# Optimization experiments

Measured on AMD Instinct MI355X. Metric: run time of the kernel, lower is better.

The kernel has to match this reference:

```python
import jax, jax.numpy as jnp
import numpy as np

D_MODEL = 1024
N_HEAD = 16
D_K = 64
D_V = 64
D_INNER = 4096
MAX_REL = 16
EPS = 1e-6


def _rel_index(length_q, length_k):
    # Shaw-style clipped relative distance matrix -> indices into embedding table
    dist = jnp.arange(length_k)[None, :] - jnp.arange(length_q)[:, None]
    return jnp.clip(dist, -MAX_REL, MAX_REL) + MAX_REL  # [Lq, Lk] in [0, 2*MAX_REL]


def _layer_norm(x, gamma, beta):
    mu = jnp.mean(x, axis=-1, keepdims=True)
    var = jnp.var(x, axis=-1, keepdims=True)
    return (x - mu) / jnp.sqrt(var + EPS) * gamma + beta


def setup_inputs() -> dict:
    key = jax.random.key(0)
    ks = jax.random.split(key, 16)
    B, L = 8, 1024
    s = 0.02
    inp = {
        "q": jax.random.normal(ks[0], (B, L, D_MODEL), jnp.float32),
        "k": jax.random.normal(ks[1], (B, L, D_MODEL), jnp.float32),
        "v": jax.random.normal(ks[2], (B, L, D_MODEL), jnp.float32),
        "wq": jax.random.normal(ks[3], (D_MODEL, D_MODEL), jnp.float32) * s,
        "bq": jnp.zeros((D_MODEL,), jnp.float32),
        "wk": jax.random.normal(ks[4], (D_MODEL, D_MODEL), jnp.float32) * s,
        "bk": jnp.zeros((D_MODEL,), jnp.float32),
        "wv": jax.random.normal(ks[5], (D_MODEL, D_MODEL), jnp.float32) * s,
        "bv": jnp.zeros((D_MODEL,), jnp.float32),
        "wfc": jax.random.normal(ks[6], (D_MODEL, D_MODEL), jnp.float32) * s,
        "bfc": jnp.zeros((D_MODEL,), jnp.float32),
        "w1": jax.random.normal(ks[7], (D_MODEL, D_INNER), jnp.float32) * s,
        "b1": jnp.zeros((D_INNER,), jnp.float32),
        "w2": jax.random.normal(ks[8], (D_INNER, D_MODEL), jnp.float32) * s,
        "b2": jnp.zeros((D_MODEL,), jnp.float32),
        "ln_g": jnp.ones((D_MODEL,), jnp.float32),
        "ln_b": jnp.zeros((D_MODEL,), jnp.float32),
        "rel_k": jax.random.normal(ks[9], (2 * MAX_REL + 1, D_K), jnp.float32) * s,
        "rel_v": jax.random.normal(ks[10], (2 * MAX_REL + 1, D_V), jnp.float32) * s,
    }
    return inp


def reference(q, k, v, wq, bq, wk, bk, wv, bv, wfc, bfc, w1, b1, w2, b2, ln_g, ln_b, rel_k, rel_v):
    B, Lq, _ = q.shape
    Lk = k.shape[1]
    residual = q

    Q = q @ wq + bq  # [B, Lq, D]
    K = k @ wk + bk
    V = v @ wv + bv

    Qh = Q.reshape(B, Lq, N_HEAD, D_K)  # [B, Lq, H, dk]
    Kh = K.reshape(B, Lk, N_HEAD, D_K)
    Vh = V.reshape(B, Lk, N_HEAD, D_V)

    # content-content scores
    attn1 = jnp.einsum("bqhd,bkhd->bhqk", Qh, Kh)
    # content-position scores (Shaw relative position)
    idx = _rel_index(Lq, Lk)  # [Lq, Lk]
    k2 = rel_k[idx]           # [Lq, Lk, dk]
    attn2 = jnp.einsum("bqhd,qkd->bhqk", Qh, k2)

    attn = (attn1 + attn2) / jnp.sqrt(jnp.float32(D_K))
    attn = jax.nn.softmax(attn, axis=-1)  # dropout = identity (eval)

    weight1 = jnp.einsum("bhqk,bkhd->bhqd", attn, Vh)
    v2 = rel_v[idx]  # [Lq, Lk, dv]
    weight2 = jnp.einsum("bhqk,qkd->bhqd", attn, v2)

    out = (weight1 + weight2).transpose(0, 2, 1, 3).reshape(B, Lq, N_HEAD * D_V)
    out = out @ wfc + bfc
    out = out + residual
    out = _layer_norm(out, ln_g, ln_b)

    residual = out
    out2 = jax.nn.relu(out @ w1 + b1) @ w2 + b2
    out = _layer_norm(out2 + residual, ln_g, ln_b)  # same LN params reused, as in source
    return out
```

## Files before the change

kernel.cpp:

```cpp
#include <hip/hip_runtime.h>
#include <stdint.h>


typedef __bf16 bf16x8 __attribute__((ext_vector_type(8)));
typedef float  f32x4  __attribute__((ext_vector_type(4)));

__device__ __forceinline__ unsigned short f2bf(float f) {
  __bf16 h = (__bf16)f;
  union { __bf16 h; unsigned short u; } x; x.h = h;
  return x.u;
}
__device__ __forceinline__ float bf2f(unsigned short h) {
  union { unsigned u; float f; } x; x.u = ((unsigned)h) << 16; return x.f;
}

__device__ __forceinline__ void gload_lds16(
    const unsigned short* g,
    __attribute__((address_space(3))) unsigned int* l) {
  __builtin_amdgcn_global_load_lds(
      (const __attribute__((address_space(1))) unsigned int*)g, l, 16, 0, 0);
}

template<int EPI>
__global__ __launch_bounds__(512, 2) void gemm_bt(
    const unsigned short* __restrict__ A,
    const unsigned short* __restrict__ Bt,
    const float* __restrict__ bias0,
    const float* __restrict__ bias1,
    const float* __restrict__ bias2,
    void* __restrict__ Cout,
    int M, int N, int K,
    size_t sA, size_t sB, size_t sC)
{
  __shared__ __align__(16) unsigned short S[3 * 24576];
  const int tid = threadIdx.x;
  const int lane = tid & 63, wv = tid >> 6;
  const int lq = lane >> 4, lm = lane & 15;
  const int wr = wv >> 2, wc = wv & 3;

  const int z = blockIdx.z;
  const float* bias = (z == 0) ? bias0 : (z == 1) ? bias1 : bias2;
  A  += (size_t)z * sA;
  Bt += (size_t)z * sB;

  const int nx = gridDim.x;
  const int nwg = nx * gridDim.y;
  int bid = blockIdx.y * nx + blockIdx.x;
  bid = (bid & 7) * (nwg >> 3) + (bid >> 3);
  const int m0 = (bid / nx) * 256, n0 = (bid % nx) * 128;

  const int srow = tid >> 3;
  const int scol = ((tid & 7) ^ (srow & 7)) * 8;
  const unsigned short* ga = A  + (size_t)(m0 + srow) * K + scol;
  const unsigned short* gb = Bt + (size_t)(n0 + srow) * K + scol;

  __attribute__((address_space(3))) unsigned int* lbase =
      (__attribute__((address_space(3))) unsigned int*)S;

  f32x4 acc[8][2] = {};

  auto stage = [&](int buf) {
    __attribute__((address_space(3))) unsigned int* lA = lbase + buf * 12288 + wv * 256;
    __attribute__((address_space(3))) unsigned int* lB = lA + 8192;
    #pragma unroll
    for (int g = 0; g < 4; ++g)
      gload_lds16(ga + (size_t)(g * 64) * K, lA + g * 2048);
    #pragma unroll
    for (int g = 0; g < 2; ++g)
      gload_lds16(gb + (size_t)(g * 64) * K, lB + g * 2048);
    ga += 64; gb += 64;
  };

  const int csw0 = ((lq ^ (lm & 7)) << 4);
  const int csw1 = csw0 ^ 64;
  const char* fa = (const char*)S + (wr * 128 + lm) * 128;
  const char* fb = (const char*)S + 32768 + (wc * 32 + lm) * 128;

  auto compute_tile = [&](int buf) {
    const char* ba = fa + buf * 49152;
    const char* bb = fb + buf * 49152;
    bf16x8 bfr[2][2];
    #pragma unroll
    for (int j = 0; j < 2; ++j) {
      bfr[j][0] = *(const bf16x8*)(bb + j * 2048 + csw0);
      bfr[j][1] = *(const bf16x8*)(bb + j * 2048 + csw1);
    }
    #pragma unroll
    for (int q = 0; q < 4; ++q) {
      bf16x8 af[2][2];
      #pragma unroll
      for (int ii = 0; ii < 2; ++ii) {
        af[ii][0] = *(const bf16x8*)(ba + (q * 2 + ii) * 2048 + csw0);
        af[ii][1] = *(const bf16x8*)(ba + (q * 2 + ii) * 2048 + csw1);
      }
      __builtin_amdgcn_s_barrier();
      __builtin_amdgcn_s_setprio(1);
      #pragma unroll
      for (int ii = 0; ii < 2; ++ii)
        #pragma unroll
        for (int j = 0; j < 2; ++j)
          #pragma unroll
          for (int kk = 0; kk < 2; ++kk)
            acc[q * 2 + ii][j] = __builtin_amdgcn_mfma_f32_16x16x32_bf16(
                af[ii][kk], bfr[j][kk], acc[q * 2 + ii][j], 0, 0, 0);
      __builtin_amdgcn_s_setprio(0);
      __builtin_amdgcn_s_barrier();
    }
  };

  const int nt = K >> 6;
  stage(0);
  stage(1);
  for (int t = 0; t < nt; ++t) {
    if (t + 1 < nt) asm volatile("s_waitcnt vmcnt(6)" ::: "memory");
    else            asm volatile("s_waitcnt vmcnt(0)" ::: "memory");
    __builtin_amdgcn_s_barrier();
    __builtin_amdgcn_sched_barrier(0);
    if (t + 2 < nt) stage((t + 2) % 3);
    compute_tile(t % 3);
  }

  #pragma unroll
  for (int i = 0; i < 8; ++i) {
    #pragma unroll
    for (int j = 0; j < 2; ++j) {
      const int col = n0 + wc * 32 + j * 16 + lm;
      const float bv = bias[col];
      #pragma unroll
      for (int r = 0; r < 4; ++r) {
        const int row = m0 + wr * 128 + i * 16 + lq * 4 + r;
        float v = acc[i][j][r] + bv;
        if (EPI == 2) v = fmaxf(v, 0.0f);
        if (EPI == 1) ((float*)Cout)[(size_t)row * N + col] = v;
        else ((unsigned short*)Cout + (size_t)z * sC)[(size_t)row * N + col] = f2bf(v);
      }
    }
  }
}

__global__ __launch_bounds__(256) void tcast(
    const float* __restrict__ in, unsigned short* __restrict__ out, int R, int C)
{
  __shared__ float tile[32][33];
  const int tx = threadIdx.x & 31, ty = threadIdx.x >> 5;
  const int r0 = blockIdx.y * 32, c0 = blockIdx.x * 32;
  #pragma unroll
  for (int s = 0; s < 4; ++s)
    tile[ty + s * 8][tx] = in[(size_t)(r0 + ty + s * 8) * C + c0 + tx];
  __syncthreads();
  #pragma unroll
  for (int s = 0; s < 4; ++s)
    out[(size_t)(c0 + ty + s * 8) * R + r0 + tx] = f2bf(tile[tx][ty + s * 8]);
}

__global__ __launch_bounds__(256) void cast4(
    const float* __restrict__ in, unsigned short* __restrict__ out, int n)
{
  int i = (blockIdx.x * 256 + threadIdx.x) * 4;
  if (i < n) {
    float4 v = *(const float4*)(in + i);
    ushort4 o;
    o.x = f2bf(v.x); o.y = f2bf(v.y); o.z = f2bf(v.z); o.w = f2bf(v.w);
    *(ushort4*)(out + i) = o;
  }
}

__global__ __launch_bounds__(256) void vtrans(
    const unsigned short* __restrict__ VP, unsigned short* __restrict__ VPT)
{
  __shared__ unsigned short tile[64 * 66];
  const int pt = blockIdx.x, h = blockIdx.y, b = blockIdx.z;
  const int tid = threadIdx.x;
  const int p = tid >> 2, c0 = (tid & 3) * 16;
  const unsigned short* src = VP + (size_t)(b * 1024 + pt * 64 + p) * 1024 + h * 64 + c0;
  union { uint4 q; unsigned int u[4]; } t0, t1;
  t0.q = *(const uint4*)src;
  t1.q = *(const uint4*)(src + 8);
  #pragma unroll
  for (int e = 0; e < 4; ++e) {
    *(unsigned int*)&tile[p * 66 + c0 + e * 2]     = t0.u[e];
    *(unsigned int*)&tile[p * 66 + c0 + 8 + e * 2] = t1.u[e];
  }
  __syncthreads();
  const int d = tid >> 2, p0 = (tid & 3) * 16;
  union { uint4 q[2]; unsigned short s[16]; } ob;
  #pragma unroll
  for (int e = 0; e < 16; ++e) ob.s[e] = tile[(p0 + e) * 66 + d];
  unsigned short* dst = VPT + ((size_t)(h * 64 + d) * 8 + b) * 1024 + pt * 64 + p0;
  *(uint4*)dst       = ob.q[0];
  *(uint4*)(dst + 8) = ob.q[1];
}

__global__ __launch_bounds__(256, 4) void attn_flash(
    const unsigned short* __restrict__ Qp,
    const unsigned short* __restrict__ Kp,
    const unsigned short* __restrict__ VPT,
    const float* __restrict__ relk,
    const float* __restrict__ relv,
    unsigned short* __restrict__ ctx)
{
  int id = (blockIdx.z * gridDim.y + blockIdx.y) * gridDim.x + blockIdx.x;
  id = (id & 7) * 256 + (id >> 3);
  const int qt = id & 15, h = (id >> 4) & 15, b = id >> 8;

  const int tid = threadIdx.x;
  const int lane = tid & 63, wv = tid >> 6;
  const int lq = lane >> 4, lm = lane & 15;

  __shared__ __align__(16) unsigned short SM[18560];
  unsigned short* Kt    = SM;
  unsigned short* Vt    = SM + 4608;
  unsigned short* Pt    = SM + 9216;
  unsigned short* RaccB = SM + 13824;
  unsigned short* qrelB = SM + 16384;
  unsigned short* relvT = SM;

  const float CE = 0.125f * 1.44269504088896340736f;

  const int tok0 = b * 1024 + qt * 64;

  for (int i = tid; i < 64 * 40; i += 256) RaccB[i] = 0;

  bf16x8 qf0, qf1;
  {
    const unsigned short* qg = Qp + (size_t)(tok0 + wv * 16 + lm) * 1024 + h * 64;
    qf0 = *(const bf16x8*)(qg + lq * 8);
    qf1 = *(const bf16x8*)(qg + 32 + lq * 8);
  }

  #pragma unroll
  for (int t = 0; t < 3; ++t) {
    const int bin = t * 16 + lm;
    union { bf16x8 v; unsigned short s[8]; } rk0, rk1;
    #pragma unroll
    for (int e = 0; e < 8; ++e) { rk0.s[e] = 0; rk1.s[e] = 0; }
    if (bin < 33) {
      const float* rp = relk + bin * 64 + lq * 8;
      #pragma unroll
      for (int e = 0; e < 8; ++e) {
        rk0.s[e] = f2bf(rp[e]);
        rk1.s[e] = f2bf(rp[32 + e]);
      }
    }
    f32x4 Sr = {};
    Sr = __builtin_amdgcn_mfma_f32_16x16x32_bf16(qf0, rk0.v, Sr, 0, 0, 0);
    Sr = __builtin_amdgcn_mfma_f32_16x16x32_bf16(qf1, rk1.v, Sr, 0, 0, 0);
    if (bin < 33) {
      #pragma unroll
      for (int r = 0; r < 4; ++r)
        qrelB[(wv * 16 + lq * 4 + r) * 34 + bin] = f2bf(Sr[r] * CE);
    }
  }
  __syncthreads();

  float q0a[4], q32a[4];
  #pragma unroll
  for (int r = 0; r < 4; ++r) {
    const int rowl = wv * 16 + lq * 4 + r;
    q0a[r]  = bf2f(qrelB[rowl * 34 + 0]);
    q32a[r] = bf2f(qrelB[rowl * 34 + 32]);
  }

  union { bf16x8 v; unsigned short s[8]; } one8;
  #pragma unroll
  for (int e = 0; e < 8; ++e) one8.s[e] = 0x3F80;

  f32x4 Oa[4] = {};
  f32x4 Rs = {};
  float r0a[4] = {0, 0, 0, 0}, r32a[4] = {0, 0, 0, 0};

  const int srow = tid >> 2, scol = (tid & 3) * 16;
  const unsigned short* kg = Kp + (size_t)(b * 1024 + srow) * 1024 + h * 64 + scol;
  const unsigned short* vg = VPT + ((size_t)(h * 64 + srow) * 8 + b) * 1024 + scol;
  const int qa0 = qt * 64 + wv * 16;

  uint4 rk0_ = *(const uint4*)(kg);
  uint4 rk1_ = *(const uint4*)(kg + 8);
  uint4 rv0_ = *(const uint4*)(vg);
  uint4 rv1_ = *(const uint4*)(vg + 8);

  for (int kt = 0; kt < 16; ++kt) {
    __syncthreads();
    *(uint4*)(Kt + srow * 72 + scol)     = rk0_;
    *(uint4*)(Kt + srow * 72 + scol + 8) = rk1_;
    *(uint4*)(Vt + srow * 72 + scol)     = rv0_;
    *(uint4*)(Vt + srow * 72 + scol + 8) = rv1_;
    if (kt < 15) {
      kg += 64 * 1024;
      vg += 64;
      rk0_ = *(const uint4*)(kg);
      rk1_ = *(const uint4*)(kg + 8);
      rv0_ = *(const uint4*)(vg);
      rv1_ = *(const uint4*)(vg + 8);
    }
    __syncthreads();

    #pragma unroll
    for (int tj = 0; tj < 4; ++tj) {
      bf16x8 kf0 = *(const bf16x8*)(Kt + (tj * 16 + lm) * 72 + lq * 8);
      bf16x8 kf1 = *(const bf16x8*)(Kt + (tj * 16 + lm) * 72 + 32 + lq * 8);
      f32x4 S = {};
      S = __builtin_amdgcn_mfma_f32_16x16x32_bf16(qf0, kf0, S, 0, 0, 0);
      S = __builtin_amdgcn_mfma_f32_16x16x32_bf16(qf1, kf1, S, 0, 0, 0);
      const int c0 = kt * 64 + tj * 16;
      if (c0 + 31 <= qa0) {
        #pragma unroll
        for (int r = 0; r < 4; ++r) {
          const float p = __builtin_amdgcn_exp2f(fmaf(S[r], CE, q0a[r]));
          r0a[r] += p;
          Pt[(wv * 16 + lq * 4 + r) * 72 + tj * 16 + lm] = f2bf(p);
        }
      } else if (c0 >= qa0 + 31) {
        #pragma unroll
        for (int r = 0; r < 4; ++r) {
          const float p = __builtin_amdgcn_exp2f(fmaf(S[r], CE, q32a[r]));
          r32a[r] += p;
          Pt[(wv * 16 + lq * 4 + r) * 72 + tj * 16 + lm] = f2bf(p);
        }
      } else {
        const int kpos = c0 + lm;
        #pragma unroll
        for (int r = 0; r < 4; ++r) {
          const int rowl = wv * 16 + lq * 4 + r;
          const int dist = kpos - (qt * 64 + rowl);
          const int bin = (dist < -16 ? 0 : (dist > 16 ? 32 : dist + 16));
          const float p =
              __builtin_amdgcn_exp2f(fmaf(S[r], CE, bf2f(qrelB[rowl * 34 + bin])));
          if (bin == 0)       r0a[r]  += p;
          else if (bin == 32) r32a[r] += p;
          else RaccB[rowl * 40 + bin] = f2bf(p);
          Pt[rowl * 72 + tj * 16 + lm] = f2bf(p);
        }
      }
    }
    bf16x8 pf0 = *(const bf16x8*)(Pt + (wv * 16 + lm) * 72 + lq * 8);
    bf16x8 pf1 = *(const bf16x8*)(Pt + (wv * 16 + lm) * 72 + 32 + lq * 8);
    Rs = __builtin_amdgcn_mfma_f32_16x16x32_bf16(pf0, one8.v, Rs, 0, 0, 0);
    Rs = __builtin_amdgcn_mfma_f32_16x16x32_bf16(pf1, one8.v, Rs, 0, 0, 0);
    #pragma unroll
    for (int dt = 0; dt < 4; ++dt) {
      bf16x8 vf0 = *(const bf16x8*)(Vt + (dt * 16 + lm) * 72 + lq * 8);
      bf16x8 vf1 = *(const bf16x8*)(Vt + (dt * 16 + lm) * 72 + 32 + lq * 8);
      Oa[dt] = __builtin_amdgcn_mfma_f32_16x16x32_bf16(pf0, vf0, Oa[dt], 0, 0, 0);
      Oa[dt] = __builtin_amdgcn_mfma_f32_16x16x32_bf16(pf1, vf1, Oa[dt], 0, 0, 0);
    }
  }

  #pragma unroll
  for (int r = 0; r < 4; ++r) {
    #pragma unroll
    for (int off = 1; off < 16; off <<= 1) {
      r0a[r]  += __shfl_xor(r0a[r],  off, 64);
      r32a[r] += __shfl_xor(r32a[r], off, 64);
    }
  }
  if (lm == 0) {
    #pragma unroll
    for (int r = 0; r < 4; ++r)
      RaccB[(wv * 16 + lq * 4 + r) * 40 + 0] = f2bf(r0a[r]);
  }
  __syncthreads();
  for (int i = tid; i < 64 * 32; i += 256) {
    const int dd = i >> 5, ss = i & 31;
    relvT[dd * 32 + ss] = f2bf(relv[ss * 64 + dd]);
  }
  __syncthreads();

  bf16x8 raf = *(const bf16x8*)(RaccB + (wv * 16 + lm) * 40 + lq * 8);
  #pragma unroll
  for (int dt = 0; dt < 4; ++dt) {
    bf16x8 rvb = *(const bf16x8*)(relvT + (dt * 16 + lm) * 32 + lq * 8);
    f32x4 O2 = {};
    O2 = __builtin_amdgcn_mfma_f32_16x16x32_bf16(raf, rvb, O2, 0, 0, 0);
    const float rv32 = relv[32 * 64 + dt * 16 + lm];
    #pragma unroll
    for (int r = 0; r < 4; ++r) {
      const int rowl = wv * 16 + lq * 4 + r;
      const float v = (Oa[dt][r] + O2[r] + r32a[r] * rv32) / Rs[r];
      ctx[(size_t)(tok0 + rowl) * 1024 + h * 64 + dt * 16 + lm] = f2bf(v);
    }
  }
}

template<bool WB>
__global__ __launch_bounds__(256) void ln_res(
    const float* __restrict__ x, const float* __restrict__ res,
    const float* __restrict__ g, const float* __restrict__ bta,
    float* __restrict__ of, unsigned short* __restrict__ ob)
{
  const int row = blockIdx.x;
  const int tid = threadIdx.x;
  __shared__ float red[8];
  const size_t base = (size_t)row * 1024 + tid * 4;
  const float4 xv = *(const float4*)(x + base);
  const float4 rv = *(const float4*)(res + base);
  float v0 = xv.x + rv.x, v1 = xv.y + rv.y, v2 = xv.z + rv.z, v3 = xv.w + rv.w;
  float s1 = v0 + v1 + v2 + v3;
  float s2 = v0 * v0 + v1 * v1 + v2 * v2 + v3 * v3;
  #pragma unroll
  for (int off = 1; off < 64; off <<= 1) {
    s1 += __shfl_xor(s1, off, 64);
    s2 += __shfl_xor(s2, off, 64);
  }
  const int wv = tid >> 6;
  if ((tid & 63) == 0) { red[wv * 2] = s1; red[wv * 2 + 1] = s2; }
  __syncthreads();
  s1 = red[0] + red[2] + red[4] + red[6];
  s2 = red[1] + red[3] + red[5] + red[7];
  const float mean = s1 * (1.f / 1024.f);
  const float var = s2 * (1.f / 1024.f) - mean * mean;
  const float rstd = rsqrtf(var + 1e-6f);
  const float4 gv = *(const float4*)(g + tid * 4);
  const float4 bv = *(const float4*)(bta + tid * 4);
  float y0 = (v0 - mean) * rstd * gv.x + bv.x;
  float y1 = (v1 - mean) * rstd * gv.y + bv.y;
  float y2 = (v2 - mean) * rstd * gv.z + bv.z;
  float y3 = (v3 - mean) * rstd * gv.w + bv.w;
  float4 yo; yo.x = y0; yo.y = y1; yo.z = y2; yo.w = y3;
  *(float4*)(of + base) = yo;
  if (WB) {
    ushort4 o;
    o.x = f2bf(y0); o.y = f2bf(y1); o.z = f2bf(y2); o.w = f2bf(y3);
    *(ushort4*)(ob + base) = o;
  }
}

extern "C" void kernel_launch(void* const* d_in, const int* in_sizes, int n_in,
                              void* d_out, int out_size, void* d_ws, size_t ws_size,
                              hipStream_t stream) {
  (void)in_sizes; (void)n_in; (void)out_size; (void)ws_size;
  const float* q    = (const float*)d_in[0];
  const float* k    = (const float*)d_in[1];
  const float* v    = (const float*)d_in[2];
  const float* wq   = (const float*)d_in[3];
  const float* bq   = (const float*)d_in[4];
  const float* wk   = (const float*)d_in[5];
  const float* bk   = (const float*)d_in[6];
  const float* wv_  = (const float*)d_in[7];
  const float* bv   = (const float*)d_in[8];
  const float* wfc  = (const float*)d_in[9];
  const float* bfc  = (const float*)d_in[10];
  const float* w1   = (const float*)d_in[11];
  const float* b1   = (const float*)d_in[12];
  const float* w2   = (const float*)d_in[13];
  const float* b2   = (const float*)d_in[14];
  const float* ln_g = (const float*)d_in[15];
  const float* ln_b = (const float*)d_in[16];
  const float* rel_k = (const float*)d_in[17];
  const float* rel_v = (const float*)d_in[18];

  char* ws = (char*)d_ws;
  const size_t MB = 1ull << 20;
  unsigned short* WQT  = (unsigned short*)(ws + 0 * MB);
  unsigned short* WKT  = (unsigned short*)(ws + 2 * MB);
  unsigned short* WVT  = (unsigned short*)(ws + 4 * MB);
  unsigned short* WFCT = (unsigned short*)(ws + 6 * MB);
  unsigned short* W1T  = (unsigned short*)(ws + 8 * MB);
  unsigned short* W2T  = (unsigned short*)(ws + 16 * MB);
  unsigned short* QP   = (unsigned short*)(ws + 24 * MB);
  unsigned short* KP   = (unsigned short*)(ws + 40 * MB);
  unsigned short* VP   = (unsigned short*)(ws + 56 * MB);
  unsigned short* QBF  = (unsigned short*)(ws + 72 * MB);
  unsigned short* KBF  = (unsigned short*)(ws + 88 * MB);
  unsigned short* VBF  = (unsigned short*)(ws + 104 * MB);
  unsigned short* VPT  = QBF;
  unsigned short* CTX  = KBF;
  float*          OTMP = (float*)(ws + 104 * MB);
  float*          X1F  = (float*)(ws + 24 * MB);
  unsigned short* X1BF = VP;
  unsigned short* HBUF = (unsigned short*)(ws + 72 * MB);
  float*          Y2   = (float*)(ws + 136 * MB);

  const dim3 blk(256);
  const dim3 gblk(512);
  const int NTOK = 8192;

  tcast<<<dim3(32, 32), blk, 0, stream>>>(wq, WQT, 1024, 1024);
  tcast<<<dim3(32, 32), blk, 0, stream>>>(wk, WKT, 1024, 1024);
  tcast<<<dim3(32, 32), blk, 0, stream>>>(wv_, WVT, 1024, 1024);
  tcast<<<dim3(32, 32), blk, 0, stream>>>(wfc, WFCT, 1024, 1024);
  tcast<<<dim3(128, 32), blk, 0, stream>>>(w1, W1T, 1024, 4096);
  tcast<<<dim3(32, 128), blk, 0, stream>>>(w2, W2T, 4096, 1024);
  cast4<<<8192, blk, 0, stream>>>(q, QBF, NTOK * 1024);
  cast4<<<8192, blk, 0, stream>>>(k, KBF, NTOK * 1024);
  cast4<<<8192, blk, 0, stream>>>(v, VBF, NTOK * 1024);

  gemm_bt<0><<<dim3(8, 32, 3), gblk, 0, stream>>>(
      QBF, WQT, bq, bk, bv, QP, NTOK, 1024, 1024,
      (size_t)8 * MB, (size_t)1 * MB, (size_t)8 * MB);

  vtrans<<<dim3(16, 16, 8), blk, 0, stream>>>(VP, VPT);

  attn_flash<<<dim3(16, 16, 8), blk, 0, stream>>>(QP, KP, VPT, rel_k, rel_v, CTX);

  gemm_bt<1><<<dim3(8, 32), gblk, 0, stream>>>(CTX, WFCT, bfc, bfc, bfc, OTMP,
                                               NTOK, 1024, 1024, 0, 0, 0);
  ln_res<true><<<8192, blk, 0, stream>>>(OTMP, q, ln_g, ln_b, X1F, X1BF);
  gemm_bt<2><<<dim3(32, 32), gblk, 0, stream>>>(X1BF, W1T, b1, b1, b1, HBUF,
                                                NTOK, 4096, 1024, 0, 0, 0);
  gemm_bt<1><<<dim3(8, 32), gblk, 0, stream>>>(HBUF, W2T, b2, b2, b2, Y2,
                                               NTOK, 1024, 4096, 0, 0, 0);
  ln_res<false><<<8192, blk, 0, stream>>>(Y2, X1F, ln_g, ln_b, (float*)d_out, nullptr);
}
```

Baseline: 608.0 us.

## Use 256x256 tiles with double buffering for the FFN up-projection GEMM

Templates the GEMM on the N tile width and uses a 256-wide N tile for the W1 GEMM (8192x4096x1024). That GEMM drops from triple to double buffering so the larger tile fits in shared memory, and the wave compute loop is reshaped to cover more N fragments per A fragment. The larger tile raises arithmetic intensity and halves the block count, at the cost of more accumulator registers and less latency hiding from the shallower pipeline.

```diff
diff --git a/kernel.cpp b/kernel.cpp
--- a/kernel.cpp
+++ b/kernel.cpp
@@ -21,7 +21,7 @@
       (const __attribute__((address_space(1))) unsigned int*)g, l, 16, 0, 0);
 }
 
-template<int EPI>
+template<int EPI, int BN>
 __global__ __launch_bounds__(512, 2) void gemm_bt(
     const unsigned short* __restrict__ A,
     const unsigned short* __restrict__ Bt,
@@ -32,7 +32,16 @@
     int M, int N, int K,
     size_t sA, size_t sB, size_t sC)
 {
-  __shared__ __align__(16) unsigned short S[3 * 24576];
+  constexpr int NJ   = BN / 64;
+  constexpr int NB   = BN / 64;
+  constexpr int NP   = NJ;
+  constexpr int MQ   = 8 / NP;
+  constexpr int NBUF = (BN == 128) ? 3 : 2;
+  constexpr int SBUF_US = 16384 + BN * 64;
+  constexpr int SBUF_DW = SBUF_US / 2;
+  constexpr int SBUF_B  = SBUF_US * 2;
+
+  __shared__ __align__(16) unsigned short S[NBUF * SBUF_US];
   const int tid = threadIdx.x;
   const int lane = tid & 63, wv = tid >> 6;
   const int lq = lane >> 4, lm = lane & 15;
@@ -47,7 +56,7 @@
   const int nwg = nx * gridDim.y;
   int bid = blockIdx.y * nx + blockIdx.x;
   bid = (bid & 7) * (nwg >> 3) + (bid >> 3);
-  const int m0 = (bid / nx) * 256, n0 = (bid % nx) * 128;
+  const int m0 = (bid / nx) * 256, n0 = (bid % nx) * BN;
 
   const int srow = tid >> 3;
   const int scol = ((tid & 7) ^ (srow & 7)) * 8;
@@ -57,16 +66,18 @@
   __attribute__((address_space(3))) unsigned int* lbase =
       (__attribute__((address_space(3))) unsigned int*)S;
 
-  f32x4 acc[8][2] = {};
+  f32x4 acc[8][NJ] = {};
 
   auto stage = [&](int buf) {
-    __attribute__((address_space(3))) unsigned int* lA = lbase + buf * 12288 + wv * 256;
-    __attribute__((address_space(3))) unsigned int* lB = lA + 8192;
+    __attribute__((address_space(3))) unsigned int* lA =
+        lbase + buf * SBUF_DW + wv * 256;
+    __attribute__((address_space(3))) unsigned int* lB = 
+        lbase + buf * SBUF_DW + 8192 + wv * 256;
     #pragma unroll
     for (int g = 0; g < 4; ++g)
       gload_lds16(ga + (size_t)(g * 64) * K, lA + g * 2048);
     #pragma unroll
-    for (int g = 0; g < 2; ++g)
+    for (int g = 0; g < NB; ++g)
       gload_lds16(gb + (size_t)(g * 64) * K, lB + g * 2048);
     ga += 64; gb += 64;
   };
@@ -74,57 +85,72 @@
   const int csw0 = ((lq ^ (lm & 7)) << 4);
   const int csw1 = csw0 ^ 64;
   const char* fa = (const char*)S + (wr * 128 + lm) * 128;
-  const char* fb = (const char*)S + 32768 + (wc * 32 + lm) * 128;
+  const char* fb = (const char*)S + 32768 + (wc * (BN / 4) + lm) * 128;
 
   auto compute_tile = [&](int buf) {
-    const char* ba = fa + buf * 49152;
-    const char* bb = fb + buf * 49152;
-    bf16x8 bfr[2][2];
-    #pragma unroll
-    for (int j = 0; j < 2; ++j) {
+    const char* ba = fa + buf * SBUF_B;
+    const char* bb = fb + buf * SBUF_B;
+    bf16x8 bfr[NJ][2];
+    #pragma unroll
+    for (int j = 0; j < NJ; ++j) {
       bfr[j][0] = *(const bf16x8*)(bb + j * 2048 + csw0);
       bfr[j][1] = *(const bf16x8*)(bb + j * 2048 + csw1);
     }
     #pragma unroll
-    for (int q = 0; q < 4; ++q) {
-      bf16x8 af[2][2];
+    for (int p = 0; p < NP; ++p) {
+      bf16x8 af[MQ][2];
       #pragma unroll
-      for (int ii = 0; ii < 2; ++ii) {
-        af[ii][0] = *(const bf16x8*)(ba + (q * 2 + ii) * 2048 + csw0);
-        af[ii][1] = *(const bf16x8*)(ba + (q * 2 + ii) * 2048 + csw1);
+      for (int ii = 0; ii < MQ; ++ii) {
+        af[ii][0] = *(const bf16x8*)(ba + (p * MQ + ii) * 2048 + csw0);
+        af[ii][1] = *(const bf16x8*)(ba + (p * MQ + ii) * 2048 + csw1);
       }
       __builtin_amdgcn_s_barrier();
       __builtin_amdgcn_s_setprio(1);
       #pragma unroll
-      for (int ii = 0; ii < 2; ++ii)
+      for (int ii = 0; ii < MQ; ++ii)
         #pragma unroll
-        for (int j = 0; j < 2; ++j)
+        for (int j = 0; j < NJ; ++j)
           #pragma unroll
           for (int kk = 0; kk < 2; ++kk)
-            acc[q * 2 + ii][j] = __builtin_amdgcn_mfma_f32_16x16x32_bf16(
-                af[ii][kk], bfr[j][kk], acc[q * 2 + ii][j], 0, 0, 0);
+            acc[p * MQ + ii][j] = __builtin_amdgcn_mfma_f32_16x16x32_bf16(
+                af[ii][kk], bfr[j][kk], acc[p * MQ + ii][j], 0, 0, 0);
       __builtin_amdgcn_s_setprio(0);
       __builtin_amdgcn_s_barrier();
     }
   };
 
   const int nt = K >> 6;
-  stage(0);
-  stage(1);
-  for (int t = 0; t < nt; ++t) {
-    if (t + 1 < nt) asm volatile("s_waitcnt vmcnt(6)" ::: "memory");
-    else            asm volatile("s_waitcnt vmcnt(0)" ::: "memory");
-    __builtin_amdgcn_s_barrier();
-    __builtin_amdgcn_sched_barrier(0);
-    if (t + 2 < nt) stage((t + 2) % 3);
-    compute_tile(t % 3);
+  if constexpr (BN == 128) {
+    stage(0);
+    stage(1);
+    for (int t = 0; t < nt; ++t) {
+      if (t + 1 < nt) asm volatile("s_waitcnt vmcnt(6)" ::: "memory");
+      else            asm volatile("s_waitcnt vmcnt(0)" ::: "memory");
+      __builtin_amdgcn_s_barrier();
+      __builtin_amdgcn_sched_barrier(0);
+      if (t + 2 < nt) stage((t + 2) % 3);
+      compute_tile(t % 3);
+    }
+  } else {
+    stage(0);
+    for (int t = 0; t < nt; ++t) {
+      if (t + 1 < nt) {
+        stage((t + 1) & 1);
+        asm volatile("s_waitcnt vmcnt(8)" ::: "memory");
+      } else {
+        asm volatile("s_waitcnt vmcnt(0)" ::: "memory");
+      }
+      __builtin_amdgcn_s_barrier();
+      __builtin_amdgcn_sched_barrier(0);
+      compute_tile(t & 1);
+    }
   }
 
   #pragma unroll
   for (int i = 0; i < 8; ++i) {
     #pragma unroll
-    for (int j = 0; j < 2; ++j) {
-      const int col = n0 + wc * 32 + j * 16 + lm;
+    for (int j = 0; j < NJ; ++j) {
+      const int col = n0 + wc * (BN / 4) + j * 16 + lm;
       const float bv = bias[col];
       #pragma unroll
       for (int r = 0; r < 4; ++r) {
@@ -485,7 +511,7 @@
   cast4<<<8192, blk, 0, stream>>>(k, KBF, NTOK * 1024);
   cast4<<<8192, blk, 0, stream>>>(v, VBF, NTOK * 1024);
 
-  gemm_bt<0><<<dim3(8, 32, 3), gblk, 0, stream>>>(
+  gemm_bt<0, 128><<<dim3(8, 32, 3), gblk, 0, stream>>>(
       QBF, WQT, bq, bk, bv, QP, NTOK, 1024, 1024,
       (size_t)8 * MB, (size_t)1 * MB, (size_t)8 * MB);
 
@@ -493,12 +519,12 @@
 
   attn_flash<<<dim3(16, 16, 8), blk, 0, stream>>>(QP, KP, VPT, rel_k, rel_v, CTX);
 
-  gemm_bt<1><<<dim3(8, 32), gblk, 0, stream>>>(CTX, WFCT, bfc, bfc, bfc, OTMP,
-                                               NTOK, 1024, 1024, 0, 0, 0);
+  gemm_bt<1, 128><<<dim3(8, 32), gblk, 0, stream>>>(CTX, WFCT, bfc, bfc, bfc, OTMP,
+                                                    NTOK, 1024, 1024, 0, 0, 0);
   ln_res<true><<<8192, blk, 0, stream>>>(OTMP, q, ln_g, ln_b, X1F, X1BF);
-  gemm_bt<2><<<dim3(32, 32), gblk, 0, stream>>>(X1BF, W1T, b1, b1, b1, HBUF,
-                                                NTOK, 4096, 1024, 0, 0, 0);
-  gemm_bt<1><<<dim3(8, 32), gblk, 0, stream>>>(HBUF, W2T, b2, b2, b2, Y2,
-                                               NTOK, 1024, 4096, 0, 0, 0);
+  gemm_bt<2, 256><<<dim3(16, 32), gblk, 0, stream>>>(X1BF, W1T, b1, b1, b1, HBUF,
+                                                     NTOK, 4096, 1024, 0, 0, 0);
+  gemm_bt<1, 128><<<dim3(8, 32), gblk, 0, stream>>>(HBUF, W2T, b2, b2, b2, Y2,
+                                                    NTOK, 1024, 4096, 0, 0, 0);
   ln_res<false><<<8192, blk, 0, stream>>>(Y2, X1F, ln_g, ln_b, (float*)d_out, nullptr);
 }
```

After: 572.0 us. 1.06x faster.
